# Performance work log

Hardware: AMD Instinct MI355X
Metric: run time of the kernel (lower is better)

## Reference

```python
import jax, jax.numpy as jnp
import numpy as np

N = 50000   # nodes
E = 200000  # edges per snapshot
T = 2       # temporal snapshots
IN = 64     # in_dim
H = 32      # h_dim
ED = 16     # edge_dim
Z = 32      # z_dim
S = 5       # neighbor samples


def setup_inputs() -> dict:
    key = jax.random.key(0)
    ks = jax.random.split(key, 20)
    g = lambda i, shape: jax.random.normal(ks[i], shape, jnp.float32) * 0.05
    return {
        "x": jax.random.normal(ks[0], (N, IN), jnp.float32),
        "ei0": jax.random.randint(ks[1], (2, E), 0, N, dtype=jnp.int32),
        "ea0": jax.random.normal(ks[2], (E, ED), jnp.float32),
        "ei1": jax.random.randint(ks[3], (2, E), 0, N, dtype=jnp.int32),
        "ea1": jax.random.normal(ks[4], (E, ED), jnp.float32),
        "idx": jnp.sort(jax.random.randint(ks[5], (N + 1,), 0, E, dtype=jnp.int32)),
        "ptr": jax.random.randint(ks[6], (E,), 0, N, dtype=jnp.int32),
        "W1": g(7, (IN, H)), "b1": jnp.zeros((H,), jnp.float32),
        "W2": g(8, (H, H)), "b2": jnp.zeros((H,), jnp.float32),
        "W3": g(9, (H, H)), "b3": jnp.zeros((H,), jnp.float32),
        "nnW1": g(10, (ED, 8)), "nnb1": jnp.zeros((8,), jnp.float32),
        "nnW2": g(11, (8, H * H)), "nnb2": jnp.zeros((H * H,), jnp.float32),
        "root": g(12, (H, H)), "cbias": jnp.zeros((H,), jnp.float32),
        "Wih": g(13, (3 * H, H)), "Whh": g(14, (3 * H, H)),
        "bih": jnp.zeros((3 * H,), jnp.float32), "bhh": jnp.zeros((3 * H,), jnp.float32),
        "Wlin": g(15, (H, Z)), "blin": jnp.zeros((Z,), jnp.float32),
        "Wdec": g(16, (Z, Z)), "bdec": jnp.zeros((Z,), jnp.float32),
    }


def _gcn(z, src, dst, W, b):
    # GCNConv with symmetric norm; self loops already in (src, dst)
    deg = jax.ops.segment_sum(jnp.ones_like(src, jnp.float32), dst, N)
    dinv = jnp.where(deg > 0, 1.0 / jnp.sqrt(jnp.maximum(deg, 1.0)), 0.0)
    h = z @ W
    msg = (dinv[src] * dinv[dst])[:, None] * h[src]
    return jax.ops.segment_sum(msg, dst, N) + b


def _nnconv(z, src, dst, ea, nnW1, nnb1, nnW2, nnb2, root, cbias):
    # edge MLP -> per-edge [H,H] weight, per-edge matvec, mean-scatter at dst
    We = (jax.nn.relu(ea @ nnW1 + nnb1) @ nnW2 + nnb2).reshape(-1, H, H)
    msg = jnp.einsum('eh,eho->eo', z[src], We)
    cnt = jax.ops.segment_sum(jnp.ones_like(src, jnp.float32), dst, N)
    agg = jax.ops.segment_sum(msg, dst, N) / jnp.maximum(cnt, 1.0)[:, None]
    return agg + z @ root + cbias


def _forward(x, ei0, ea0, ei1, ea1, idx, ptr,
             W1, b1, W2, b2, W3, b3, nnW1, nnb1, nnW2, nnb2, root, cbias,
             Wih, Whh, bih, bhh, Wlin, blin, Wdec, bdec):
    loops = jnp.arange(N, dtype=ei0.dtype)

    def snap(ei, ea):
        src, dst = ei[0], ei[1]
        ssl = jnp.concatenate([src, loops])
        dsl = jnp.concatenate([dst, loops])
        z = _gcn(x, ssl, dsl, W1, b1)                 # c1 (no act)
        z = jax.nn.relu(_gcn(z, ssl, dsl, W2, b2))    # c2 + relu (dropout=eval)
        z = jax.nn.relu(_gcn(z, ssl, dsl, W3, b3))    # c3 + relu
        return jnp.tanh(_nnconv(z, src, dst, ea, nnW1, nnb1, nnW2, nnb2, root, cbias))

    zs = jnp.stack([snap(ei0, ea0), snap(ei1, ea1)], axis=1)  # [N, T, H]

    # nn.GRU(batch_first=False) on [N, T, H]: scans over NODE axis, batch=T
    def step(h, xt):
        gi = xt @ Wih.T + bih
        gh = h @ Whh.T + bhh
        ir, iz, inn = jnp.split(gi, 3, axis=-1)
        hr, hz, hn = jnp.split(gh, 3, axis=-1)
        r = jax.nn.sigmoid(ir + hr)
        u = jax.nn.sigmoid(iz + hz)
        n = jnp.tanh(inn + r * hn)
        hnew = (1.0 - u) * n + u * h
        return hnew, hnew

    _, ys = jax.lax.scan(step, jnp.zeros((T, H), jnp.float32), zs)
    out = ys @ Wlin + blin  # [N, T, Z]

    # sample_z: uniform sample of S neighbors (with replacement) from CSR (idx, ptr)
    deg = (idx[1:] - idx[:-1]).astype(jnp.float32)  # [N]
    key = jax.random.key(42)
    res = []
    for t in range(T):
        u = jax.random.uniform(jax.random.fold_in(key, t), (N, S))
        j = jnp.floor(u * deg[:, None]).astype(idx.dtype)
        pos = jnp.clip(idx[:-1, None] + j, 0, E - 1)
        nb = ptr[pos]                               # [N, S] sampled neighbors
        zt = out[:, t, :]
        ag = (zt[nb].sum(axis=1) + zt) / (S + 1.0)
        ag = jnp.where((deg > 0)[:, None], ag, zt)  # no neighbors -> identity
        res.append(jax.nn.softmax(ag @ Wdec + bdec, axis=1))
    return jnp.stack(res)  # [T, N, Z]


def reference(x, ei0, ea0, ei1, ea1, idx, ptr,
              W1, b1, W2, b2, W3, b3, nnW1, nnb1, nnW2, nnb2, root, cbias,
              Wih, Whh, bih, bhh, Wlin, blin, Wdec, bdec):
    return _forward(x, ei0, ea0, ei1, ea1, idx, ptr,
                    W1, b1, W2, b2, W3, b3, nnW1, nnb1, nnW2, nnb2, root, cbias,
                    Wih, Whh, bih, bhh, Wlin, blin, Wdec, bdec)
```

## Files before the change

kernel.cpp:

```cpp
#include <hip/hip_runtime.h>
#include <stdint.h>

constexpr int NN = 50000;
constexpr int EE = 200000;
constexpr int N2 = 2*NN;
constexpr int E2 = 2*EE;
constexpr int GRU_WARM   = 24;
constexpr int GRU_CHUNKS = 2048;
constexpr int NB_SCAN = (N2 + 511) / 512;

#define DEVI __device__ __forceinline__

typedef float f32x2 __attribute__((ext_vector_type(2)));

DEVI uint32_t rotl32(uint32_t v, int d){ return (v<<d)|(v>>(32-d)); }

#define TFR(r) { x0 += x1; x1 = rotl32(x1, r); x1 ^= x0; }
DEVI void tf2x32(uint32_t k0, uint32_t k1, uint32_t x0, uint32_t x1,
                 uint32_t& o0, uint32_t& o1){
  uint32_t ks2 = k0 ^ k1 ^ 0x1BD11BDAu;
  x0 += k0; x1 += k1;
  TFR(13) TFR(15) TFR(26) TFR(6)
  x0 += k1;  x1 += ks2 + 1u;
  TFR(17) TFR(29) TFR(16) TFR(24)
  x0 += ks2; x1 += k0 + 2u;
  TFR(13) TFR(15) TFR(26) TFR(6)
  x0 += k0;  x1 += k1 + 3u;
  TFR(17) TFR(29) TFR(16) TFR(24)
  x0 += k1;  x1 += ks2 + 4u;
  TFR(13) TFR(15) TFR(26) TFR(6)
  x0 += ks2; x1 += k0 + 5u;
  o0 = x0; o1 = x1;
}

DEVI unsigned short bfr(float f){
  uint32_t u = __float_as_uint(f);
  return (unsigned short)((u + 0x7fffu + ((u >> 16) & 1u)) >> 16);
}
DEVI float bfi(unsigned short h){ return __uint_as_float(((uint32_t)h) << 16); }

DEVI uint32_t pk4f8(float a, float b, float c, float d){
  int r = 0;
  r = __builtin_amdgcn_cvt_pk_fp8_f32(a, b, r, false);
  r = __builtin_amdgcn_cvt_pk_fp8_f32(c, d, r, true);
  return (uint32_t)r;
}
DEVI float4 upk4f8(uint32_t u){
  f32x2 lo = __builtin_amdgcn_cvt_pk_f32_fp8((int)u, false);
  f32x2 hi = __builtin_amdgcn_cvt_pk_f32_fp8((int)u, true);
  return make_float4(lo.x, lo.y, hi.x, hi.y);
}
constexpr float P8SCALE = 64.0f;

template<int K, int ACTIN, int TRW, int EPI>
__global__ __launch_bounds__(256) void tgemm_k(
    const float* __restrict__ X, const float* __restrict__ Wg,
    const float* __restrict__ Bv, float* __restrict__ Y, float* __restrict__ Y2,
    const float* __restrict__ dinvB, unsigned short* __restrict__ Ybf,
    int rows, int Mt, int wld){
  __shared__ float xt[K*132];
  __shared__ float wl[K*32];
  const int gr = blockIdx.x, gy = blockIdx.y;
  #pragma unroll
  for (int p=0; p<K/8; p++){
    int flat = p*256 + threadIdx.x;
    int row  = flat / (K/4);
    int kq   = flat % (K/4);
    int grow = min(gr*128 + row, rows-1);
    float4 v = *(const float4*)(X + (size_t)grow*K + kq*4);
    if (ACTIN){ v.x=fmaxf(v.x,0.f); v.y=fmaxf(v.y,0.f); v.z=fmaxf(v.z,0.f); v.w=fmaxf(v.w,0.f); }
    xt[(kq*4+0)*132 + row] = v.x;
    xt[(kq*4+1)*132 + row] = v.y;
    xt[(kq*4+2)*132 + row] = v.z;
    xt[(kq*4+3)*132 + row] = v.w;
  }
  for (int i=threadIdx.x; i<K*32; i+=256){
    int k = i >> 5, c = i & 31;
    wl[i] = TRW ? Wg[(size_t)(gy*32+c)*wld + k] : Wg[(size_t)k*wld + gy*32 + c];
  }
  __syncthreads();
  const int tr4 = (threadIdx.x & 31) << 2;
  const int tc4 = (threadIdx.x >> 5) << 2;
  float acc[4][4] = {};
  #pragma unroll 8
  for (int k=0; k<K; k++){
    const float4 xv = *(const float4*)(xt + k*132 + tr4);
    const float4 wv = *(const float4*)(wl + (k<<5) + tc4);
    acc[0][0]=fmaf(xv.x,wv.x,acc[0][0]); acc[0][1]=fmaf(xv.x,wv.y,acc[0][1]);
    acc[0][2]=fmaf(xv.x,wv.z,acc[0][2]); acc[0][3]=fmaf(xv.x,wv.w,acc[0][3]);
    acc[1][0]=fmaf(xv.y,wv.x,acc[1][0]); acc[1][1]=fmaf(xv.y,wv.y,acc[1][1]);
    acc[1][2]=fmaf(xv.y,wv.z,acc[1][2]); acc[1][3]=fmaf(xv.y,wv.w,acc[1][3]);
    acc[2][0]=fmaf(xv.z,wv.x,acc[2][0]); acc[2][1]=fmaf(xv.z,wv.y,acc[2][1]);
    acc[2][2]=fmaf(xv.z,wv.z,acc[2][2]); acc[2][3]=fmaf(xv.z,wv.w,acc[2][3]);
    acc[3][0]=fmaf(xv.w,wv.x,acc[3][0]); acc[3][1]=fmaf(xv.w,wv.y,acc[3][1]);
    acc[3][2]=fmaf(xv.w,wv.z,acc[3][2]); acc[3][3]=fmaf(xv.w,wv.w,acc[3][3]);
  }
  const int cbase = gy*32 + tc4;
  float b4[4] = {0,0,0,0};
  if (Bv){ b4[0]=Bv[cbase]; b4[1]=Bv[cbase+1]; b4[2]=Bv[cbase+2]; b4[3]=Bv[cbase+3]; }
  #pragma unroll
  for (int i=0;i<4;i++){
    int r = gr*128 + tr4 + i;
    if (r >= rows) break;
    if (EPI == 0){
      float4 o = { acc[i][0]+b4[0], acc[i][1]+b4[1], acc[i][2]+b4[2], acc[i][3]+b4[3] };
      *(float4*)(Y + (size_t)r*Mt + cbase) = o;
    } else if (EPI == 1){
      float dv = dinvB[r];
      float4 hs = { dv*acc[i][0], dv*acc[i][1], dv*acc[i][2], dv*acc[i][3] };
      ushort4 u = { bfr(hs.x), bfr(hs.y), bfr(hs.z), bfr(hs.w) };
      *(ushort4*)(Ybf + ((size_t)r<<5) + tc4) = u;
      float4 o = { b4[0]+dv*hs.x, b4[1]+dv*hs.y, b4[2]+dv*hs.z, b4[3]+dv*hs.w };
      *(float4*)(Y2 + ((size_t)r<<5) + tc4) = o;
    } else if (EPI == 2){
      ushort4 u = { bfr(acc[i][0]+b4[0]), bfr(acc[i][1]+b4[1]),
                    bfr(acc[i][2]+b4[2]), bfr(acc[i][3]+b4[3]) };
      *(ushort4*)(Ybf + (size_t)r*Mt + cbase) = u;
    } else {
      #pragma unroll
      for (int s=0;s<2;s++){
        int rr = r*2+s;
        float dv = dinvB[rr];
        float4 hs = { dv*acc[i][0], dv*acc[i][1], dv*acc[i][2], dv*acc[i][3] };
        ushort4 u = { bfr(hs.x), bfr(hs.y), bfr(hs.z), bfr(hs.w) };
        *(ushort4*)(Ybf + ((size_t)rr<<5) + tc4) = u;
        float4 o = { b4[0]+dv*hs.x, b4[1]+dv*hs.y, b4[2]+dv*hs.z, b4[3]+dv*hs.w };
        *(float4*)(Y2 + ((size_t)rr<<5) + tc4) = o;
      }
    }
  }
}

__global__ __launch_bounds__(256) void pgemm_k(const float* __restrict__ X,
    const float* __restrict__ Wbig2, unsigned char* __restrict__ P8,
    float* __restrict__ R, int rows){
  __shared__ float xt[32*132];
  __shared__ float wl[32*320];
  const int gr = blockIdx.x;
  #pragma unroll
  for (int p=0; p<4; p++){
    int flat = p*256 + threadIdx.x;
    int row = flat >> 3, kq = flat & 7;
    int grow = min(gr*128 + row, rows-1);
    float4 v = *(const float4*)(X + (size_t)grow*32 + kq*4);
    v.x=fmaxf(v.x,0.f); v.y=fmaxf(v.y,0.f); v.z=fmaxf(v.z,0.f); v.w=fmaxf(v.w,0.f);
    xt[(kq*4+0)*132 + row] = v.x;
    xt[(kq*4+1)*132 + row] = v.y;
    xt[(kq*4+2)*132 + row] = v.z;
    xt[(kq*4+3)*132 + row] = v.w;
  }
  for (int i=threadIdx.x; i<(32*320/4); i+=256)
    ((float4*)wl)[i] = ((const float4*)Wbig2)[i];
  __syncthreads();
  const int tr4 = (threadIdx.x & 31) << 2;
  const int tc4 = (threadIdx.x >> 5) << 2;
  for (int gy=0; gy<10; gy++){
    float acc[4][4] = {};
    #pragma unroll 8
    for (int k=0; k<32; k++){
      const float4 xv = *(const float4*)(xt + k*132 + tr4);
      const float4 wv = *(const float4*)(wl + k*320 + gy*32 + tc4);
      acc[0][0]=fmaf(xv.x,wv.x,acc[0][0]); acc[0][1]=fmaf(xv.x,wv.y,acc[0][1]);
      acc[0][2]=fmaf(xv.x,wv.z,acc[0][2]); acc[0][3]=fmaf(xv.x,wv.w,acc[0][3]);
      acc[1][0]=fmaf(xv.y,wv.x,acc[1][0]); acc[1][1]=fmaf(xv.y,wv.y,acc[1][1]);
      acc[1][2]=fmaf(xv.y,wv.z,acc[1][2]); acc[1][3]=fmaf(xv.y,wv.w,acc[1][3]);
      acc[2][0]=fmaf(xv.z,wv.x,acc[2][0]); acc[2][1]=fmaf(xv.z,wv.y,acc[2][1]);
      acc[2][2]=fmaf(xv.z,wv.z,acc[2][2]); acc[2][3]=fmaf(xv.z,wv.w,acc[2][3]);
      acc[3][0]=fmaf(xv.w,wv.x,acc[3][0]); acc[3][1]=fmaf(xv.w,wv.y,acc[3][1]);
      acc[3][2]=fmaf(xv.w,wv.z,acc[3][2]); acc[3][3]=fmaf(xv.w,wv.w,acc[3][3]);
    }
    #pragma unroll
    for (int i=0;i<4;i++){
      int r = gr*128 + tr4 + i;
      if (r >= rows) break;
      if (gy < 9){
        uint32_t u = pk4f8(acc[i][0]*P8SCALE, acc[i][1]*P8SCALE,
                           acc[i][2]*P8SCALE, acc[i][3]*P8SCALE);
        *(uint32_t*)(P8 + (size_t)r*288 + gy*32 + tc4) = u;
      } else {
        float4 o = { acc[i][0], acc[i][1], acc[i][2], acc[i][3] };
        *(float4*)(R + ((size_t)r<<5) + tc4) = o;
      }
    }
  }
}

__global__ void zsfin_k(float* __restrict__ R, const float* __restrict__ agg,
                        const float* __restrict__ degB, const float* __restrict__ cbias){
  int t = blockIdx.x*blockDim.x + threadIdx.x;
  if (t >= N2*8) return;
  int n = t >> 3, q = (t & 7) << 2;
  float inv = (1.0f/P8SCALE) / fmaxf(degB[n], 1.0f);
  const float4 ag = *(const float4*)(agg + ((size_t)n<<5) + q);
  float4 v = *(const float4*)(R + ((size_t)n<<5) + q);
  const float* cb = cbias + q;
  v.x = v.x + cb[0] + ag.x*inv;
  v.y = v.y + cb[1] + ag.y*inv;
  v.z = v.z + cb[2] + ag.z*inv;
  v.w = v.w + cb[3] + ag.w*inv;
  float4 o;
  o.x = 1.0f - 2.0f/(__expf(2.0f*v.x)+1.0f);
  o.y = 1.0f - 2.0f/(__expf(2.0f*v.y)+1.0f);
  o.z = 1.0f - 2.0f/(__expf(2.0f*v.z)+1.0f);
  o.w = 1.0f - 2.0f/(__expf(2.0f*v.w)+1.0f);
  *(float4*)(R + ((size_t)n<<5) + q) = o;
}

__global__ void cnt_k(const int* __restrict__ ei0, const int* __restrict__ ei1,
                      int* __restrict__ cnt){
  int t = blockIdx.x*blockDim.x + threadIdx.x;
  if (t >= E2) return;
  int s = t >= EE;
  const int* ei = s ? ei1 : ei0;
  int e = t - s*EE;
  atomicAdd(cnt + ei[EE + e]*2 + s, 1);
}

__global__ __launch_bounds__(512) void scan1_k(const int* __restrict__ cnt,
                                               int* __restrict__ loc, int* __restrict__ bsum){
  int tid = threadIdx.x;
  int i = blockIdx.x*512 + tid;
  int v = (i < N2) ? cnt[i] : 0;
  int lane = tid & 63, w = tid >> 6;
  int s = v;
  #pragma unroll
  for (int d=1; d<64; d<<=1){ int o = __shfl_up(s, d); if (lane >= d) s += o; }
  __shared__ int wsum[8];
  if (lane == 63) wsum[w] = s;
  __syncthreads();
  int add = 0;
  #pragma unroll
  for (int k=0;k<8;k++) if (k < w) add += wsum[k];
  if (i < N2) loc[i] = add + s - v;
  if (tid == 511) bsum[blockIdx.x] = add + s;
}

__global__ __launch_bounds__(256) void scan2_k(int* __restrict__ bsum){
  int tid = threadIdx.x;
  int v = (tid < NB_SCAN) ? bsum[tid] : 0;
  int lane = tid & 63, w = tid >> 6;
  int s = v;
  #pragma unroll
  for (int d=1; d<64; d<<=1){ int o = __shfl_up(s, d); if (lane >= d) s += o; }
  __shared__ int wsum[4];
  if (lane == 63) wsum[w] = s;
  __syncthreads();
  int add = 0;
  #pragma unroll
  for (int k=0;k<4;k++) if (k < w) add += wsum[k];
  if (tid < NB_SCAN) bsum[tid] = add + s - v;
}

__global__ void scan3_k(const int* __restrict__ bsum, int* __restrict__ cursor,
                        int* __restrict__ rowptr, const int* __restrict__ cnt,
                        float* __restrict__ dinvB, float* __restrict__ degB){
  int i = blockIdx.x*blockDim.x + threadIdx.x;
  if (i < N2){
    int r = cursor[i] + bsum[i >> 9];
    rowptr[i] = r; cursor[i] = r;
    float c = (float)cnt[i];
    degB[i] = c; dinvB[i] = rsqrtf(c + 1.0f);
  }
  if (i == N2) rowptr[N2] = E2;
}

__global__ void fill_k(const int* __restrict__ ei0, const int* __restrict__ ei1,
                       int* __restrict__ cursor,
                       int* __restrict__ csr_src, int* __restrict__ csr_eid){
  int t = blockIdx.x*blockDim.x + threadIdx.x;
  if (t >= E2) return;
  int s = t >= EE;
  const int* ei = s ? ei1 : ei0;
  int e = t - s*EE;
  int d = ei[EE + e];
  int slot = atomicAdd(cursor + d*2 + s, 1);
  csr_src[slot] = ei[e]*2 + s;
  csr_eid[slot] = e;
}

__global__ __launch_bounds__(256) void temlp_k(const float* __restrict__ ea0,
    const float* __restrict__ ea1, const float* __restrict__ nnW1,
    const float* __restrict__ nnb1, unsigned short* __restrict__ tb){
  __shared__ float wt[136];
  for (int i=threadIdx.x; i<136; i+=256)
    wt[i] = (i < 128) ? nnW1[(i & 15)*8 + (i >> 4)] : nnb1[i - 128];
  __syncthreads();
  int t = blockIdx.x*256 + threadIdx.x;
  if (t >= E2) return;
  int s = t >= EE;
  const float* ea = s ? ea1 : ea0;
  int e = t - s*EE;
  const float4 a0 = *(const float4*)(ea + (size_t)e*16);
  const float4 a1 = *(const float4*)(ea + (size_t)e*16 + 4);
  const float4 a2 = *(const float4*)(ea + (size_t)e*16 + 8);
  const float4 a3 = *(const float4*)(ea + (size_t)e*16 + 12);
  unsigned short o8[8];
  #pragma unroll
  for (int m=0;m<8;m++){
    const float* wc = wt + m*16;
    float v = wt[128+m];
    v = fmaf(a0.x,wc[0], fmaf(a0.y,wc[1], fmaf(a0.z,wc[2], fmaf(a0.w,wc[3], v))));
    v = fmaf(a1.x,wc[4], fmaf(a1.y,wc[5], fmaf(a1.z,wc[6], fmaf(a1.w,wc[7], v))));
    v = fmaf(a2.x,wc[8], fmaf(a2.y,wc[9], fmaf(a2.z,wc[10],fmaf(a2.w,wc[11],v))));
    v = fmaf(a3.x,wc[12],fmaf(a3.y,wc[13],fmaf(a3.z,wc[14],fmaf(a3.w,wc[15],v))));
    o8[m] = bfr(fmaxf(v, 0.0f));
  }
  ushort4* tp = (ushort4*)(tb + (size_t)t*8);
  tp[0] = make_ushort4(o8[0],o8[1],o8[2],o8[3]);
  tp[1] = make_ushort4(o8[4],o8[5],o8[6],o8[7]);
}

__global__ __launch_bounds__(256) void gcngath_k(const unsigned short* __restrict__ hs,
    const float* __restrict__ dinvB, const int* __restrict__ rowptr,
    const int* __restrict__ csr_src, float* __restrict__ out){
  int t = blockIdx.x*256 + threadIdx.x;
  int n = t >> 3;
  if (n >= N2) return;
  int q = (t & 7) << 2;
  int b = rowptr[n], e = rowptr[n+1];
  float4 acc = {0,0,0,0};
  int p = b;
  for (; p + 2 <= e; p += 2){
    int s0 = csr_src[p], s1 = csr_src[p+1];
    ushort4 h0 = *(const ushort4*)(hs + ((size_t)s0<<5) + q);
    ushort4 h1 = *(const ushort4*)(hs + ((size_t)s1<<5) + q);
    acc.x += bfi(h0.x) + bfi(h1.x);
    acc.y += bfi(h0.y) + bfi(h1.y);
    acc.z += bfi(h0.z) + bfi(h1.z);
    acc.w += bfi(h0.w) + bfi(h1.w);
  }
  if (p < e){
    int s0 = csr_src[p];
    ushort4 h0 = *(const ushort4*)(hs + ((size_t)s0<<5) + q);
    acc.x += bfi(h0.x); acc.y += bfi(h0.y); acc.z += bfi(h0.z); acc.w += bfi(h0.w);
  }
  float dv = dinvB[n];
  float4 o = *(float4*)(out + ((size_t)n<<5) + q);
  o.x += dv*acc.x; o.y += dv*acc.y; o.z += dv*acc.z; o.w += dv*acc.w;
  *(float4*)(out + ((size_t)n<<5) + q) = o;
}

__global__ __launch_bounds__(256) void nngath_k(const unsigned char* __restrict__ P8,
    const unsigned short* __restrict__ tb,
    const int* __restrict__ rowptr, const int* __restrict__ csr_src,
    const int* __restrict__ csr_eid, float* __restrict__ agg){
  int t = blockIdx.x*256 + threadIdx.x;
  int n = t >> 3;
  if (n >= N2) return;
  int lane8 = threadIdx.x & 7;
  int ob = lane8 << 2;
  int sEE = (n & 1) ? EE : 0;
  int b = rowptr[n], e = rowptr[n+1];
  float4 acc = {0,0,0,0};
  int p = b;
  for (; p + 2 <= e; p += 2){
    int v0 = csr_src[p],   e0 = csr_eid[p];
    int v1 = csr_src[p+1], e1 = csr_eid[p+1];
    const unsigned char* pr0 = P8 + (size_t)v0*288 + ob;
    const unsigned char* pr1 = P8 + (size_t)v1*288 + ob;
    uint32_t u0[9], u1[9];
    #pragma unroll
    for (int k=0;k<9;k++) u0[k] = *(const uint32_t*)(pr0 + k*32);
    #pragma unroll
    for (int k=0;k<9;k++) u1[k] = *(const uint32_t*)(pr1 + k*32);
    ushort4 ta0 = *(const ushort4*)(tb + (size_t)(sEE + e0)*8);
    ushort4 tb0 = *(const ushort4*)(tb + (size_t)(sEE + e0)*8 + 4);
    ushort4 ta1 = *(const ushort4*)(tb + (size_t)(sEE + e1)*8);
    ushort4 tb1 = *(const ushort4*)(tb + (size_t)(sEE + e1)*8 + 4);
    float tc0[8] = { bfi(ta0.x),bfi(ta0.y),bfi(ta0.z),bfi(ta0.w),
                     bfi(tb0.x),bfi(tb0.y),bfi(tb0.z),bfi(tb0.w) };
    float tc1[8] = { bfi(ta1.x),bfi(ta1.y),bfi(ta1.z),bfi(ta1.w),
                     bfi(tb1.x),bfi(tb1.y),bfi(tb1.z),bfi(tb1.w) };
    float4 m0 = upk4f8(u0[0]);
    float4 m1 = upk4f8(u1[0]);
    #pragma unroll
    for (int k=0;k<8;k++){
      float4 q0 = upk4f8(u0[k+1]);
      m0.x = fmaf(tc0[k], q0.x, m0.x);
      m0.y = fmaf(tc0[k], q0.y, m0.y);
      m0.z = fmaf(tc0[k], q0.z, m0.z);
      m0.w = fmaf(tc0[k], q0.w, m0.w);
      float4 q1 = upk4f8(u1[k+1]);
      m1.x = fmaf(tc1[k], q1.x, m1.x);
      m1.y = fmaf(tc1[k], q1.y, m1.y);
      m1.z = fmaf(tc1[k], q1.z, m1.z);
      m1.w = fmaf(tc1[k], q1.w, m1.w);
    }
    acc.x += m0.x + m1.x; acc.y += m0.y + m1.y;
    acc.z += m0.z + m1.z; acc.w += m0.w + m1.w;
  }
  if (p < e){
    int v0 = csr_src[p], e0 = csr_eid[p];
    const unsigned char* pr0 = P8 + (size_t)v0*288 + ob;
    uint32_t u0[9];
    #pragma unroll
    for (int k=0;k<9;k++) u0[k] = *(const uint32_t*)(pr0 + k*32);
    ushort4 ta0 = *(const ushort4*)(tb + (size_t)(sEE + e0)*8);
    ushort4 tb0 = *(const ushort4*)(tb + (size_t)(sEE + e0)*8 + 4);
    float tc0[8] = { bfi(ta0.x),bfi(ta0.y),bfi(ta0.z),bfi(ta0.w),
                     bfi(tb0.x),bfi(tb0.y),bfi(tb0.z),bfi(tb0.w) };
    float4 m0 = upk4f8(u0[0]);
    #pragma unroll
    for (int k=0;k<8;k++){
      float4 q0 = upk4f8(u0[k+1]);
      m0.x = fmaf(tc0[k], q0.x, m0.x);
      m0.y = fmaf(tc0[k], q0.y, m0.y);
      m0.z = fmaf(tc0[k], q0.z, m0.z);
      m0.w = fmaf(tc0[k], q0.w, m0.w);
    }
    acc.x += m0.x; acc.y += m0.y; acc.z += m0.z; acc.w += m0.w;
  }
  *(float4*)(agg + ((size_t)n<<5) + ob) = acc;
}

__global__ void wprep_k(const float* __restrict__ nnW2, const float* __restrict__ nnb2,
                        const float* __restrict__ root,
                        const float* __restrict__ Wlin, const float* __restrict__ blin,
                        const float* __restrict__ Wdec, const float* __restrict__ bdec,
                        float* __restrict__ Wbig2, float* __restrict__ Wp,
                        float* __restrict__ bp){
  int i = blockIdx.x*blockDim.x + threadIdx.x;
  if (i < 32*320){
    int j = i / 320, m = i - j*320;
    float v;
    if (m >= 288)      v = root[j*32 + (m - 288)];
    else { int k = m >> 5, o = m & 31;
           v = (k == 0) ? nnb2[j*32 + o] : nnW2[(size_t)(k-1)*1024 + j*32 + o]; }
    Wbig2[i] = v;
  } else if (i < 32*320 + 1024){
    int ii = i - 32*320;
    int k = ii >> 5, m = ii & 31;
    float s = 0.0f;
    #pragma unroll 8
    for (int j=0;j<32;j++) s = fmaf(Wlin[k*32+j], Wdec[j*32+m], s);
    Wp[ii] = s;
  } else if (i < 32*320 + 1056){
    int m = i - 32*320 - 1024;
    float s = bdec[m];
    #pragma unroll 8
    for (int j=0;j<32;j++) s = fmaf(blin[j], Wdec[j*32+m], s);
    bp[m] = s;
  }
}

__global__ __launch_bounds__(64) __attribute__((amdgpu_waves_per_eu(1, 2)))
void gru_k(const unsigned short* __restrict__ gi16,
    const float* __restrict__ Whh, const float* __restrict__ bhh,
    float* __restrict__ ys, int L){
  __shared__ float hl[64];
  int lane = threadIdx.x;
  int j = lane & 31, t = lane >> 5;
  int start = blockIdx.x * L;
  if (start >= NN) return;
  int end = min(start + L, NN);
  int n0 = max(0, start - GRU_WARM);
  float wr[32], wz[32], wn[32];
  #pragma unroll
  for (int k=0;k<32;k++) wr[k] = Whh[j*32 + k];
  #pragma unroll
  for (int k=0;k<32;k++) wz[k] = Whh[(32+j)*32 + k];
  #pragma unroll
  for (int k=0;k<32;k++) wn[k] = Whh[(64+j)*32 + k];
  #pragma unroll
  for (int k=0;k<32;k++)
    asm volatile("" : "+v"(wr[k]), "+v"(wz[k]), "+v"(wn[k]));
  float br = bhh[j], bz = bhh[32+j], bn = bhh[64+j];
  float h = 0.0f;
  hl[lane] = 0.0f;
  const unsigned short* g0 = gi16 + ((size_t)n0*2 + t)*96;
  float c0 = bfi(g0[j]), c1 = bfi(g0[32+j]), c2 = bfi(g0[64+j]);
  const float* hb = hl + (t << 5);
  for (int n = n0; n < end; n++){
    int np = (n+1 < end) ? n+1 : n;
    const unsigned short* gp = gi16 + ((size_t)np*2 + t)*96;
    float p0 = bfi(gp[j]), p1 = bfi(gp[32+j]), p2 = bfi(gp[64+j]);
    float ar = br, az = bz, an = bn;
    #pragma unroll
    for (int kk=0; kk<8; kk++){
      const float4 h4 = *(const float4*)(hb + (kk<<2));
      ar = fmaf(h4.x, wr[kk*4+0], ar); az = fmaf(h4.x, wz[kk*4+0], az); an = fmaf(h4.x, wn[kk*4+0], an);
      ar = fmaf(h4.y, wr[kk*4+1], ar); az = fmaf(h4.y, wz[kk*4+1], az); an = fmaf(h4.y, wn[kk*4+1], an);
      ar = fmaf(h4.z, wr[kk*4+2], ar); az = fmaf(h4.z, wz[kk*4+2], az); an = fmaf(h4.z, wn[kk*4+2], an);
      ar = fmaf(h4.w, wr[kk*4+3], ar); az = fmaf(h4.w, wz[kk*4+3], az); an = fmaf(h4.w, wn[kk*4+3], an);
    }
    float r = 1.0f/(1.0f + __expf(-(c0+ar)));
    float u = 1.0f/(1.0f + __expf(-(c1+az)));
    float pre = c2 + r*an;
    float e2 = __expf(2.0f*pre);
    float nn2 = 1.0f - 2.0f/(e2 + 1.0f);
    h = (1.0f-u)*nn2 + u*h;
    hl[lane] = h;
    if (n >= start) ys[((size_t)n << 6) + lane] = h;
    c0 = p0; c1 = p1; c2 = p2;
  }
}

__global__ __launch_bounds__(256) void final_k(const unsigned short* __restrict__ Lp,
    const int* __restrict__ idx, const int* __restrict__ ptr,
    float* __restrict__ dout){
  int grp = blockIdx.x*8 + (threadIdx.x >> 5);
  if (grp >= N2) return;
  int o = threadIdx.x & 31;
  int lane = threadIdx.x & 63;
  int t = (grp >= NN) ? 1 : 0;
  int n = grp - (t ? NN : 0);
  int i0 = idx[n], i1 = idx[n+1];
  float degf = (float)(i1 - i0);
  int nb = 0;
  {
    uint32_t fk0, fk1;
    tf2x32(0u, 42u, 0u, (uint32_t)t, fk0, fk1);
    int sidx = (o < 5) ? o : 4;
    uint32_t b = (uint32_t)(n*5 + sidx);
    bool hi = (b >= 125000u);
    uint32_t pair = hi ? (b - 125000u) : b;
    uint32_t r0, r1;
    tf2x32(fk0, fk1, pair, pair + 125000u, r0, r1);
    uint32_t bits = hi ? r1 : r0;
    float u = __uint_as_float((bits >> 9) | 0x3f800000u) - 1.0f;
    int jj = (int)floorf(u * degf);
    int pos = i0 + jj;
    pos = min(max(pos, 0), EE - 1);
    nb = ptr[pos];
  }
  float lo = bfi(Lp[((size_t)(n*2 + t) << 5) + o]);
  if (degf > 0.0f){
    float ssum = lo;
    #pragma unroll
    for (int s5=0;s5<5;s5++){
      int ns = __shfl(nb, (lane & 32) | s5);
      ssum += bfi(Lp[((size_t)(ns*2 + t) << 5) + o]);
    }
    lo = ssum * (1.0f/6.0f);
  }
  float m = lo;
  #pragma unroll
  for (int d5=16; d5>0; d5>>=1) m = fmaxf(m, __shfl_xor(m, d5));
  float ex = __expf(lo - m);
  float sum = ex;
  #pragma unroll
  for (int d5=16; d5>0; d5>>=1) sum += __shfl_xor(sum, d5);
  dout[((size_t)t*NN + n)*32 + o] = ex / sum;
}

static inline int g256(int n){ return (n + 255) / 256; }

extern "C" void kernel_launch(void* const* d_in, const int* in_sizes, int n_in,
                              void* d_out, int out_size, void* d_ws, size_t ws_size,
                              hipStream_t stream){
  const float* x    = (const float*)d_in[0];
  const int*   ei0  = (const int*)  d_in[1];
  const float* ea0  = (const float*)d_in[2];
  const int*   ei1  = (const int*)  d_in[3];
  const float* ea1  = (const float*)d_in[4];
  const int*   idx  = (const int*)  d_in[5];
  const int*   ptr  = (const int*)  d_in[6];
  const float* W1   = (const float*)d_in[7];
  const float* b1   = (const float*)d_in[8];
  const float* W2   = (const float*)d_in[9];
  const float* b2   = (const float*)d_in[10];
  const float* W3   = (const float*)d_in[11];
  const float* b3   = (const float*)d_in[12];
  const float* nnW1 = (const float*)d_in[13];
  const float* nnb1 = (const float*)d_in[14];
  const float* nnW2 = (const float*)d_in[15];
  const float* nnb2 = (const float*)d_in[16];
  const float* root = (const float*)d_in[17];
  const float* cbias= (const float*)d_in[18];
  const float* Wih  = (const float*)d_in[19];
  const float* Whh  = (const float*)d_in[20];
  const float* bih  = (const float*)d_in[21];
  const float* bhh  = (const float*)d_in[22];
  const float* Wlin = (const float*)d_in[23];
  const float* blin = (const float*)d_in[24];
  const float* Wdec = (const float*)d_in[25];
  const float* bdec = (const float*)d_in[26];

  float* ws = (float*)d_ws;
  size_t off = 0;
  float* degB = ws + off; off += N2;
  float* dinvB= ws + off; off += N2;
  float* Wbig2= ws + off; off += 32*320;
  float* Wp   = ws + off; off += 1024;
  float* bp   = ws + off; off += 32;
  int*   ib   = (int*)(ws + off); off += 1200000;
  unsigned short* tbuf = (unsigned short*)(ws + off); off += 1600000;
  float* A    = ws + off; off += (size_t)N2*32;
  float* B    = ws + off; off += (size_t)N2*32;
  float* C    = ws + off; off += (size_t)N2*32;
  float* D    = ws + off; off += (size_t)N2*80;
  unsigned short* hbf = (unsigned short*)D;
  unsigned char*  P8  = (unsigned char*)D;
  unsigned short* gi16 = (unsigned short*)B;
  float* ys   = D;
  unsigned short* Lp = (unsigned short*)A;

  int* cnt     = ib;
  int* rowptr  = ib + N2;
  int* cursor  = ib + 2*N2 + 1;
  int* bsum    = ib + 3*N2 + 1;
  int* csr_src = ib + 3*N2 + 1 + 256;
  int* csr_eid = csr_src + E2;

  const dim3 gN1(( NN + 127)/128, 1);
  const dim3 gB1((N2 + 127)/128, 1), gB3((N2 + 127)/128, 3);

  wprep_k<<<g256(32*320 + 1056), 256, 0, stream>>>(nnW2, nnb2, root, Wlin, blin,
                                                   Wdec, bdec, Wbig2, Wp, bp);
  temlp_k<<<g256(E2), 256, 0, stream>>>(ea0, ea1, nnW1, nnb1, tbuf);

  hipMemsetAsync(cnt, 0, N2*sizeof(int), stream);
  cnt_k <<<g256(E2), 256, 0, stream>>>(ei0, ei1, cnt);
  scan1_k<<<NB_SCAN, 512, 0, stream>>>(cnt, cursor, bsum);
  scan2_k<<<1, 256, 0, stream>>>(bsum);
  scan3_k<<<g256(N2+1), 256, 0, stream>>>(bsum, cursor, rowptr, cnt, dinvB, degB);
  fill_k<<<g256(E2), 256, 0, stream>>>(ei0, ei1, cursor, csr_src, csr_eid);

  tgemm_k<64,0,0,4><<<gN1, 256, 0, stream>>>(x, W1, b1, nullptr, B, dinvB, hbf, NN, 32, 32);
  gcngath_k<<<g256(N2*8), 256, 0, stream>>>(hbf, dinvB, rowptr, csr_src, B);
  tgemm_k<32,0,0,1><<<gB1, 256, 0, stream>>>(B, W2, b2, nullptr, C, dinvB, hbf, N2, 32, 32);
  gcngath_k<<<g256(N2*8), 256, 0, stream>>>(hbf, dinvB, rowptr, csr_src, C);
  tgemm_k<32,1,0,1><<<gB1, 256, 0, stream>>>(C, W3, b3, nullptr, B, dinvB, hbf, N2, 32, 32);
  gcngath_k<<<g256(N2*8), 256, 0, stream>>>(hbf, dinvB, rowptr, csr_src, B);
  pgemm_k<<<gB1, 256, 0, stream>>>(B, Wbig2, P8, A, N2);
  nngath_k<<<g256(N2*8), 256, 0, stream>>>(P8, tbuf, rowptr, csr_src, csr_eid, C);
  zsfin_k<<<g256(N2*8), 256, 0, stream>>>(A, C, degB, cbias);
  tgemm_k<32,0,1,2><<<gB3, 256, 0, stream>>>(A, Wih, bih, nullptr, nullptr, nullptr, gi16, N2, 96, 32);
  int L = (NN + GRU_CHUNKS - 1) / GRU_CHUNKS;
  gru_k<<<GRU_CHUNKS, 64, 0, stream>>>(gi16, Whh, bhh, ys, L);
  tgemm_k<32,0,0,2><<<gB1, 256, 0, stream>>>(ys, Wp, bp, nullptr, nullptr, nullptr, Lp, N2, 32, 32);
  final_k<<<(N2 + 7)/8, 256, 0, stream>>>(Lp, idx, ptr, (float*)d_out);
}
```

Measured before the change: 313.7 us.

## Fuse NNConv finalize into gather, split pgemm columns, add dedicated GI GEMM

Folds the zsfin elementwise finalize (root term, bias, mean scaling, tanh) into the NNConv gather kernel, removing one launch and a round trip of the aggregate buffer through memory. The per-edge weight GEMM is split into two column halves over a second grid dimension, doubling block count and halving per-block shared weight storage. The input-gate GEMM switches from the generic 3-way gridded tgemm to a dedicated kernel that computes all 96 gate columns per block from a transposed shared copy of Wih. Risks include reloading the X tile twice in pgemm and slower uncoalesced transposed weight loads.

After: 301.4 us. 3.9% less time.

```diff
diff --git a/kernel.cpp b/kernel.cpp
--- a/kernel.cpp
+++ b/kernel.cpp
@@ -135,8 +135,8 @@
     const float* __restrict__ Wbig2, unsigned char* __restrict__ P8,
     float* __restrict__ R, int rows){
   __shared__ float xt[32*132];
-  __shared__ float wl[32*320];
-  const int gr = blockIdx.x;
+  __shared__ float wl[32*160];
+  const int gr = blockIdx.x, gh = blockIdx.y;
   #pragma unroll
   for (int p=0; p<4; p++){
     int flat = p*256 + threadIdx.x;
@@ -149,17 +149,20 @@
     xt[(kq*4+2)*132 + row] = v.z;
     xt[(kq*4+3)*132 + row] = v.w;
   }
-  for (int i=threadIdx.x; i<(32*320/4); i+=256)
-    ((float4*)wl)[i] = ((const float4*)Wbig2)[i];
+  for (int i=threadIdx.x; i<(32*160/4); i+=256){
+    int k = i / 40, c4 = i - k*40;
+    ((float4*)wl)[i] = ((const float4*)Wbig2)[k*80 + gh*40 + c4];
+  }
   __syncthreads();
   const int tr4 = (threadIdx.x & 31) << 2;
   const int tc4 = (threadIdx.x >> 5) << 2;
-  for (int gy=0; gy<10; gy++){
+  for (int g=0; g<5; g++){
+    int sg = gh*5 + g;
     float acc[4][4] = {};
     #pragma unroll 8
     for (int k=0; k<32; k++){
       const float4 xv = *(const float4*)(xt + k*132 + tr4);
-      const float4 wv = *(const float4*)(wl + k*320 + gy*32 + tc4);
+      const float4 wv = *(const float4*)(wl + k*160 + g*32 + tc4);
       acc[0][0]=fmaf(xv.x,wv.x,acc[0][0]); acc[0][1]=fmaf(xv.x,wv.y,acc[0][1]);
       acc[0][2]=fmaf(xv.x,wv.z,acc[0][2]); acc[0][3]=fmaf(xv.x,wv.w,acc[0][3]);
       acc[1][0]=fmaf(xv.y,wv.x,acc[1][0]); acc[1][1]=fmaf(xv.y,wv.y,acc[1][1]);
@@ -173,10 +176,10 @@
     for (int i=0;i<4;i++){
       int r = gr*128 + tr4 + i;
       if (r >= rows) break;
-      if (gy < 9){
+      if (sg < 9){
         uint32_t u = pk4f8(acc[i][0]*P8SCALE, acc[i][1]*P8SCALE,
                            acc[i][2]*P8SCALE, acc[i][3]*P8SCALE);
-        *(uint32_t*)(P8 + (size_t)r*288 + gy*32 + tc4) = u;
+        *(uint32_t*)(P8 + (size_t)r*288 + sg*32 + tc4) = u;
       } else {
         float4 o = { acc[i][0], acc[i][1], acc[i][2], acc[i][3] };
         *(float4*)(R + ((size_t)r<<5) + tc4) = o;
@@ -185,25 +188,56 @@
   }
 }
 
-__global__ void zsfin_k(float* __restrict__ R, const float* __restrict__ agg,
-                        const float* __restrict__ degB, const float* __restrict__ cbias){
-  int t = blockIdx.x*blockDim.x + threadIdx.x;
-  if (t >= N2*8) return;
-  int n = t >> 3, q = (t & 7) << 2;
-  float inv = (1.0f/P8SCALE) / fmaxf(degB[n], 1.0f);
-  const float4 ag = *(const float4*)(agg + ((size_t)n<<5) + q);
-  float4 v = *(const float4*)(R + ((size_t)n<<5) + q);
-  const float* cb = cbias + q;
-  v.x = v.x + cb[0] + ag.x*inv;
-  v.y = v.y + cb[1] + ag.y*inv;
-  v.z = v.z + cb[2] + ag.z*inv;
-  v.w = v.w + cb[3] + ag.w*inv;
-  float4 o;
-  o.x = 1.0f - 2.0f/(__expf(2.0f*v.x)+1.0f);
-  o.y = 1.0f - 2.0f/(__expf(2.0f*v.y)+1.0f);
-  o.z = 1.0f - 2.0f/(__expf(2.0f*v.z)+1.0f);
-  o.w = 1.0f - 2.0f/(__expf(2.0f*v.w)+1.0f);
-  *(float4*)(R + ((size_t)n<<5) + q) = o;
+__global__ __launch_bounds__(256) void gigemm_k(const float* __restrict__ X,
+    const float* __restrict__ Wih, const float* __restrict__ bih,
+    unsigned short* __restrict__ gi16, int rows){
+  __shared__ float xt[32*132];
+  __shared__ float wl[32*96];
+  const int gr = blockIdx.x;
+  #pragma unroll
+  for (int p=0; p<4; p++){
+    int flat = p*256 + threadIdx.x;
+    int row = flat >> 3, kq = flat & 7;
+    int grow = min(gr*128 + row, rows-1);
+    float4 v = *(const float4*)(X + (size_t)grow*32 + kq*4);
+    xt[(kq*4+0)*132 + row] = v.x;
+    xt[(kq*4+1)*132 + row] = v.y;
+    xt[(kq*4+2)*132 + row] = v.z;
+    xt[(kq*4+3)*132 + row] = v.w;
+  }
+  for (int i=threadIdx.x; i<32*96; i+=256){
+    int k = i / 96, c = i - k*96;
+    wl[i] = Wih[(size_t)c*32 + k];
+  }
+  __syncthreads();
+  const int tr4 = (threadIdx.x & 31) << 2;
+  const int tc4 = (threadIdx.x >> 5) << 2;
+  for (int g=0; g<3; g++){
+    float acc[4][4] = {};
+    #pragma unroll 8
+    for (int k=0; k<32; k++){
+      const float4 xv = *(const float4*)(xt + k*132 + tr4);
+      const float4 wv = *(const float4*)(wl + k*96 + g*32 + tc4);
+      acc[0][0]=fmaf(xv.x,wv.x,acc[0][0]); acc[0][1]=fmaf(xv.x,wv.y,acc[0][1]);
+      acc[0][2]=fmaf(xv.x,wv.z,acc[0][2]); acc[0][3]=fmaf(xv.x,wv.w,acc[0][3]);
+      acc[1][0]=fmaf(xv.y,wv.x,acc[1][0]); acc[1][1]=fmaf(xv.y,wv.y,acc[1][1]);
+      acc[1][2]=fmaf(xv.y,wv.z,acc[1][2]); acc[1][3]=fmaf(xv.y,wv.w,acc[1][3]);
+      acc[2][0]=fmaf(xv.z,wv.x,acc[2][0]); acc[2][1]=fmaf(xv.z,wv.y,acc[2][1]);
+      acc[2][2]=fmaf(xv.z,wv.z,acc[2][2]); acc[2][3]=fmaf(xv.z,wv.w,acc[2][3]);
+      acc[3][0]=fmaf(xv.w,wv.x,acc[3][0]); acc[3][1]=fmaf(xv.w,wv.y,acc[3][1]);
+      acc[3][2]=fmaf(xv.w,wv.z,acc[3][2]); acc[3][3]=fmaf(xv.w,wv.w,acc[3][3]);
+    }
+    const int cbase = g*32 + tc4;
+    const float4 b4 = *(const float4*)(bih + cbase);
+    #pragma unroll
+    for (int i=0;i<4;i++){
+      int r = gr*128 + tr4 + i;
+      if (r >= rows) break;
+      ushort4 u = { bfr(acc[i][0]+b4.x), bfr(acc[i][1]+b4.y),
+                    bfr(acc[i][2]+b4.z), bfr(acc[i][3]+b4.w) };
+      *(ushort4*)(gi16 + (size_t)r*96 + cbase) = u;
+    }
+  }
 }
 
 __global__ void cnt_k(const int* __restrict__ ei0, const int* __restrict__ ei1,
@@ -343,7 +377,8 @@
 __global__ __launch_bounds__(256) void nngath_k(const unsigned char* __restrict__ P8,
     const unsigned short* __restrict__ tb,
     const int* __restrict__ rowptr, const int* __restrict__ csr_src,
-    const int* __restrict__ csr_eid, float* __restrict__ agg){
+    const int* __restrict__ csr_eid, float* __restrict__ R,
+    const float* __restrict__ degB, const float* __restrict__ cbias){
   int t = blockIdx.x*256 + threadIdx.x;
   int n = t >> 3;
   if (n >= N2) return;
@@ -410,7 +445,20 @@
     }
     acc.x += m0.x; acc.y += m0.y; acc.z += m0.z; acc.w += m0.w;
   }
-  *(float4*)(agg + ((size_t)n<<5) + ob) = acc;
+  float inv = (1.0f/P8SCALE) / fmaxf(degB[n], 1.0f);
+  float4 rv = *(const float4*)(R + ((size_t)n<<5) + ob);
+  const float4 cb = *(const float4*)(cbias + ob);
+  float4 v;
+  v.x = rv.x + cb.x + acc.x*inv;
+  v.y = rv.y + cb.y + acc.y*inv;
+  v.z = rv.z + cb.z + acc.z*inv;
+  v.w = rv.w + cb.w + acc.w*inv;
+  float4 o;
+  o.x = 1.0f - 2.0f/(__expf(2.0f*v.x)+1.0f);
+  o.y = 1.0f - 2.0f/(__expf(2.0f*v.y)+1.0f);
+  o.z = 1.0f - 2.0f/(__expf(2.0f*v.z)+1.0f);
+  o.w = 1.0f - 2.0f/(__expf(2.0f*v.w)+1.0f);
+  *(float4*)(R + ((size_t)n<<5) + ob) = o;
 }
 
 __global__ void wprep_k(const float* __restrict__ nnW2, const float* __restrict__ nnb2,
@@ -603,7 +651,8 @@
   int* csr_eid = csr_src + E2;
 
   const dim3 gN1(( NN + 127)/128, 1);
-  const dim3 gB1((N2 + 127)/128, 1), gB3((N2 + 127)/128, 3);
+  const dim3 gB1((N2 + 127)/128, 1);
+  const dim3 gP2((N2 + 127)/128, 2);
 
   wprep_k<<<g256(32*320 + 1056), 256, 0, stream>>>(nnW2, nnb2, root, Wlin, blin,
                                                    Wdec, bdec, Wbig2, Wp, bp);
@@ -622,10 +671,9 @@
   gcngath_k<<<g256(N2*8), 256, 0, stream>>>(hbf, dinvB, rowptr, csr_src, C);
   tgemm_k<32,1,0,1><<<gB1, 256, 0, stream>>>(C, W3, b3, nullptr, B, dinvB, hbf, N2, 32, 32);
   gcngath_k<<<g256(N2*8), 256, 0, stream>>>(hbf, dinvB, rowptr, csr_src, B);
-  pgemm_k<<<gB1, 256, 0, stream>>>(B, Wbig2, P8, A, N2);
-  nngath_k<<<g256(N2*8), 256, 0, stream>>>(P8, tbuf, rowptr, csr_src, csr_eid, C);
-  zsfin_k<<<g256(N2*8), 256, 0, stream>>>(A, C, degB, cbias);
-  tgemm_k<32,0,1,2><<<gB3, 256, 0, stream>>>(A, Wih, bih, nullptr, nullptr, nullptr, gi16, N2, 96, 32);
+  pgemm_k<<<gP2, 256, 0, stream>>>(B, Wbig2, P8, A, N2);
+  nngath_k<<<g256(N2*8), 256, 0, stream>>>(P8, tbuf, rowptr, csr_src, csr_eid, A, degB, cbias);
+  gigemm_k<<<gB1, 256, 0, stream>>>(A, Wih, bih, gi16, N2);
   int L = (NN + GRU_CHUNKS - 1) / GRU_CHUNKS;
   gru_k<<<GRU_CHUNKS, 64, 0, stream>>>(gi16, Whh, bhh, ys, L);
   tgemm_k<32,0,0,2><<<gB1, 256, 0, stream>>>(ys, Wp, bp, nullptr, nullptr, nullptr, Lp, N2, 32, 32);
```
